# Kernel tuning notes

Measured on AMD Instinct MI355X. Metric: run time of the kernel, lower is better.

## Reference

```python
import jax, jax.numpy as jnp
import numpy as np

N_NODES = 100000
N_EDGES = 1600000
NFEAT = 64
NHID = 64
NCLASS = 16


def setup_inputs() -> dict:
    key = jax.random.key(0)
    k_x, k_e, k_w1, k_b1, k_w2, k_b2 = jax.random.split(key, 6)
    x = jax.random.normal(k_x, (N_NODES, NFEAT), dtype=jnp.float32)
    edge_index = jax.random.randint(k_e, (2, N_EDGES), 0, N_NODES, dtype=jnp.int64)
    # Glorot-ish init for the GIN update MLP
    W1 = jax.random.normal(k_w1, (NFEAT, NHID), dtype=jnp.float32) * (1.0 / np.sqrt(NFEAT))
    b1 = jnp.zeros((NHID,), dtype=jnp.float32)
    W2 = jax.random.normal(k_w2, (NHID, NCLASS), dtype=jnp.float32) * (1.0 / np.sqrt(NHID))
    b2 = jnp.zeros((NCLASS,), dtype=jnp.float32)
    eps = jnp.float32(0.0)  # train_eps=True, initialized to 0
    return {"x": x, "edge_index": edge_index, "eps": eps,
            "W1": W1, "b1": b1, "W2": W2, "b2": b2}


def reference(x, edge_index, eps, W1, b1, W2, b2):
    # GINConv: out = MLP((1 + eps) * x + sum_{j in N(i)} x_j)
    src = edge_index[0]  # message source nodes
    dst = edge_index[1]  # aggregation targets (source_to_target flow)
    agg = jax.ops.segment_sum(x[src], dst, num_segments=x.shape[0])  # [N, F]
    h = (1.0 + eps) * x + agg
    # MLP([nfeat, nhid, nclass]): Linear -> ReLU -> (dropout=identity in eval) -> Linear
    h = jax.nn.relu(h @ W1 + b1)
    return h @ W2 + b2
```

## Files before the change

### kernel.cpp

```cpp
#include <hip/hip_runtime.h>
#include <hip/hip_bf16.h>
#include <hip/hip_fp16.h>


#define NFEAT 64
#define NHID 64
#define NCLASS 16

#define BNODES 128
#define PCAP 2560
#define MAXBUCK 1024
#define PT 512
#define PEPT 8
#define FT 512
#define SEPT 5

__global__ __launch_bounds__(256) void k_tofp16(
    const float4* __restrict__ x4, uint2* __restrict__ xh2, int n16)
{
    int i = blockIdx.x * 256 + threadIdx.x;
    if (i >= n16) return;
    float4 v = x4[i];
    __half2 a = __floats2half2_rn(v.x, v.y);
    __half2 b = __floats2half2_rn(v.z, v.w);
    xh2[i] = make_uint2(*(unsigned*)&a, *(unsigned*)&b);
}

__global__ __launch_bounds__(512) void k_init(int* __restrict__ cursor, int nbuck)
{
    int t = blockIdx.x * 512 + threadIdx.x;
    if (t < nbuck) cursor[t] = t * PCAP;
}

__global__ __launch_bounds__(PT) void k_part(
    const int* __restrict__ ei, int* __restrict__ cursor,
    int* __restrict__ dsts, int n_edges, int nbuck)
{
    __shared__ int lcnt[MAXBUCK];
    __shared__ int sbase[MAXBUCK];
    int tid = threadIdx.x;
    for (int i = tid; i < nbuck; i += PT) lcnt[i] = 0;
    __syncthreads();

    int e0 = blockIdx.x * (PT * PEPT);
    int bk[PEPT], rk[PEPT], pk[PEPT];
    #pragma unroll
    for (int k = 0; k < PEPT; ++k) {
        int e = e0 + k * PT + tid;
        if (e < n_edges) {
            int src = ei[e];
            int dst = ei[n_edges + e];
            int b = dst >> 7;
            bk[k] = b;
            pk[k] = (src << 7) | (dst & 127);
            rk[k] = atomicAdd(&lcnt[b], 1);
        } else bk[k] = -1;
    }
    __syncthreads();
    for (int i = tid; i < nbuck; i += PT)
        sbase[i] = lcnt[i] ? atomicAdd(&cursor[i], lcnt[i]) : 0;
    __syncthreads();
    #pragma unroll
    for (int k = 0; k < PEPT; ++k)
        if (bk[k] >= 0) dsts[sbase[bk[k]] + rk[k]] = pk[k];
}

__global__ __launch_bounds__(FT) void k_fused(
    const uint2* __restrict__ xh2,
    const float4* __restrict__ x4,
    const int* __restrict__ dsts,
    const int* __restrict__ cursor,
    const float* __restrict__ eps_p,
    const float* __restrict__ W1,
    const float* __restrict__ b1,
    const float* __restrict__ W2,
    const float* __restrict__ b2,
    float* __restrict__ out,
    int n_nodes)
{
    __shared__ float sW1[NFEAT * NHID];
    __shared__ float sW2[NHID * 17];
    __shared__ float sb1[NHID];
    __shared__ float sb2[NCLASS];
    __shared__ int   sSrc[PCAP];
    __shared__ int   sCnt[BNODES];
    __shared__ int   sOff[BNODES];
    __shared__ float sh0[32][68];
    __shared__ float sh1[32][68];

    int tid = threadIdx.x;
    int lane = tid & 63, wave = tid >> 6;

    for (int i = tid; i < NFEAT * NHID; i += FT) sW1[i] = W1[i];
    for (int i = tid; i < NHID * NCLASS; i += FT) sW2[(i >> 4) * 17 + (i & 15)] = W2[i];
    if (tid < NHID) sb1[tid] = b1[tid];
    if (tid < NCLASS) sb2[tid] = b2[tid];
    if (tid < BNODES) sCnt[tid] = 0;
    __syncthreads();

    int b = blockIdx.x;
    int gin = b * PCAP;
    int s = cursor[b] - gin;

    int dk[SEPT], rk[SEPT], sk[SEPT];
    #pragma unroll
    for (int k = 0; k < SEPT; ++k) {
        int i = k * FT + tid;
        if (i < s) {
            int p = dsts[gin + i];
            int d = p & 127;
            dk[k] = d;
            sk[k] = p >> 7;
            rk[k] = atomicAdd(&sCnt[d], 1);
        } else dk[k] = -1;
    }
    __syncthreads();
    if (wave == 0) {
        int c0 = sCnt[lane * 2], c1 = sCnt[lane * 2 + 1];
        int p1 = c0, p2 = p1 + c1;
        int ss = p2;
        #pragma unroll
        for (int o = 1; o < 64; o <<= 1) {
            int u = __shfl_up(ss, o);
            if (lane >= o) ss += u;
        }
        int base = ss - p2;
        sOff[lane * 2] = base;
        sOff[lane * 2 + 1] = base + p1;
    }
    __syncthreads();
    #pragma unroll
    for (int k = 0; k < SEPT; ++k)
        if (dk[k] >= 0) sSrc[sOff[dk[k]] + rk[k]] = sk[k];
    __syncthreads();

    float eps1 = 1.0f + eps_p[0];
    int q = lane >> 4;
    int f = lane & 15;
    int rloc = wave * 4 + q;

    #pragma unroll
    for (int pp = 0; pp < 4; ++pp) {
        int nloc = pp * 32 + rloc;
        int node = b * BNODES + nloc;
        bool valid = node < n_nodes;
        int start = sOff[nloc];
        int cntn = sCnt[nloc];

        int dmax = cntn;
        dmax = max(dmax, __shfl_xor(dmax, 16));
        dmax = max(dmax, __shfl_xor(dmax, 32));

        float4 acc = make_float4(0.f, 0.f, 0.f, 0.f);
        for (int base = 0; base < dmax; base += 16) {
            #pragma unroll
            for (int t = 0; t < 16; ++t) {
                int o = base + t;
                int idx = (o < cntn) ? sSrc[start + o] : -1;
                if (idx >= 0) {
                    uint2 hv = xh2[(size_t)idx * 8 + (f >> 1)];
                    unsigned u = (f & 1) ? hv.y : hv.x;
                    (void)u;
                }
            }
            break;
        }
        acc = make_float4(0.f, 0.f, 0.f, 0.f);
        const uint2* xr = xh2;
        for (int base = 0; base < dmax; base += 16) {
            #pragma unroll
            for (int t = 0; t < 16; ++t) {
                int o = base + t;
                int idx = (o < cntn) ? sSrc[start + o] : -1;
                if (idx >= 0) {
                    uint2 hv = xr[(size_t)idx * 16 + f];
                    __half2 ha = *(__half2*)&hv.x;
                    __half2 hb = *(__half2*)&hv.y;
                    float2 fa = __half22float2(ha);
                    float2 fb = __half22float2(hb);
                    acc.x += fa.x; acc.y += fa.y; acc.z += fb.x; acc.w += fb.y;
                }
            }
        }
        if (valid) {
            float4 xs = x4[(size_t)node * 16 + f];
            acc.x += eps1 * xs.x; acc.y += eps1 * xs.y;
            acc.z += eps1 * xs.z; acc.w += eps1 * xs.w;
        }
        *(float4*)&sh0[rloc][f * 4] = acc;

        int r = wave * 4;
        float a0 = sb1[lane], a1 = a0, a2 = a0, a3 = a0;
        #pragma unroll
        for (int kk = 0; kk < 16; ++kk) {
            float4 h0 = *(const float4*)&sh0[r + 0][kk * 4];
            float4 h1v = *(const float4*)&sh0[r + 1][kk * 4];
            float4 h2 = *(const float4*)&sh0[r + 2][kk * 4];
            float4 h3 = *(const float4*)&sh0[r + 3][kk * 4];
            #pragma unroll
            for (int i = 0; i < 4; ++i) {
                float w = sW1[(kk * 4 + i) * NHID + lane];
                a0 += ((const float*)&h0)[i] * w;
                a1 += ((const float*)&h1v)[i] * w;
                a2 += ((const float*)&h2)[i] * w;
                a3 += ((const float*)&h3)[i] * w;
            }
        }
        sh1[r + 0][lane] = fmaxf(a0, 0.f);
        sh1[r + 1][lane] = fmaxf(a1, 0.f);
        sh1[r + 2][lane] = fmaxf(a2, 0.f);
        sh1[r + 3][lane] = fmaxf(a3, 0.f);

        float o2 = sb2[f];
        #pragma unroll
        for (int jj = 0; jj < 16; ++jj) {
            float4 hv = *(const float4*)&sh1[rloc][jj * 4];
            o2 += hv.x * sW2[(jj * 4 + 0) * 17 + f];
            o2 += hv.y * sW2[(jj * 4 + 1) * 17 + f];
            o2 += hv.z * sW2[(jj * 4 + 2) * 17 + f];
            o2 += hv.w * sW2[(jj * 4 + 3) * 17 + f];
        }
        if (valid) out[(size_t)node * NCLASS + f] = o2;
    }
}

extern "C" void kernel_launch(void* const* d_in, const int* in_sizes, int n_in,
                              void* d_out, int out_size, void* d_ws, size_t ws_size,
                              hipStream_t stream) {
    const float* x   = (const float*)d_in[0];
    const int*   ei  = (const int*)d_in[1];
    const float* eps = (const float*)d_in[2];
    const float* W1  = (const float*)d_in[3];
    const float* b1  = (const float*)d_in[4];
    const float* W2  = (const float*)d_in[5];
    const float* b2  = (const float*)d_in[6];
    float* out = (float*)d_out;

    int n_nodes = in_sizes[0] / NFEAT;
    int n_edges = in_sizes[1] / 2;
    int nbuck = (n_nodes + BNODES - 1) / BNODES;

    char* ws = (char*)d_ws;
    int*   cursor = (int*)ws;
    int*   dsts   = (int*)(ws + 4096);
    size_t o_xh   = 4096 + (size_t)nbuck * PCAP * 4;
    uint2* xh2    = (uint2*)(ws + o_xh);

    int n16 = n_nodes * 16;
    k_tofp16<<<(n16 + 255) / 256, 256, 0, stream>>>((const float4*)x, xh2, n16);
    k_init<<<(nbuck + 511) / 512, 512, 0, stream>>>(cursor, nbuck);
    k_part<<<(n_edges + PT * PEPT - 1) / (PT * PEPT), PT, 0, stream>>>(
        ei, cursor, dsts, n_edges, nbuck);
    k_fused<<<nbuck, FT, 0, stream>>>(
        xh2, (const float4*)x, dsts, cursor, eps, W1, b1, W2, b2, out, n_nodes);
}
```

Before: 210.2 us.

## Replace per-node CSR sort in LDS with shared-memory atomic accumulation

```diff
diff --git a/kernel.cpp b/kernel.cpp
--- a/kernel.cpp
+++ b/kernel.cpp
@@ -7,13 +7,13 @@
 #define NHID 64
 #define NCLASS 16
 
-#define BNODES 128
-#define PCAP 2560
-#define MAXBUCK 1024
+#define BSH 6
+#define BNODES 64
+#define PCAP 1536
+#define MAXBUCK 2048
 #define PT 512
-#define PEPT 8
+#define PEPT 16
 #define FT 512
-#define SEPT 5
 
 __global__ __launch_bounds__(256) void k_tofp16(
     const float4* __restrict__ x4, uint2* __restrict__ xh2, int n16)
@@ -50,9 +50,9 @@
         if (e < n_edges) {
             int src = ei[e];
             int dst = ei[n_edges + e];
-            int b = dst >> 7;
+            int b = dst >> BSH;
             bk[k] = b;
-            pk[k] = (src << 7) | (dst & 127);
+            pk[k] = (src << BSH) | (dst & (BNODES - 1));
             rk[k] = atomicAdd(&lcnt[b], 1);
         } else bk[k] = -1;
     }
@@ -82,121 +82,74 @@
     __shared__ float sW2[NHID * 17];
     __shared__ float sb1[NHID];
     __shared__ float sb2[NCLASS];
-    __shared__ int   sSrc[PCAP];
-    __shared__ int   sCnt[BNODES];
-    __shared__ int   sOff[BNODES];
-    __shared__ float sh0[32][68];
+    __shared__ __align__(16) float accF[BNODES][NFEAT];
     __shared__ float sh1[32][68];
 
     int tid = threadIdx.x;
     int lane = tid & 63, wave = tid >> 6;
+    int b = blockIdx.x;
+    int nbase = b * BNODES;
 
     for (int i = tid; i < NFEAT * NHID; i += FT) sW1[i] = W1[i];
     for (int i = tid; i < NHID * NCLASS; i += FT) sW2[(i >> 4) * 17 + (i & 15)] = W2[i];
     if (tid < NHID) sb1[tid] = b1[tid];
     if (tid < NCLASS) sb2[tid] = b2[tid];
-    if (tid < BNODES) sCnt[tid] = 0;
-    __syncthreads();
-
-    int b = blockIdx.x;
+
+    float eps1 = 1.0f + eps_p[0];
+
+    #pragma unroll
+    for (int it = 0; it < 2; ++it) {
+        int idx = it * FT + tid;
+        int node = idx >> 4, f = idx & 15;
+        float4 v = make_float4(0.f, 0.f, 0.f, 0.f);
+        if (nbase + node < n_nodes) v = x4[(size_t)(nbase + node) * 16 + f];
+        float4 w = make_float4(eps1 * v.x, eps1 * v.y, eps1 * v.z, eps1 * v.w);
+        *(float4*)&accF[node][f * 4] = w;
+    }
+    __syncthreads();
+
     int gin = b * PCAP;
     int s = cursor[b] - gin;
-
-    int dk[SEPT], rk[SEPT], sk[SEPT];
-    #pragma unroll
-    for (int k = 0; k < SEPT; ++k) {
-        int i = k * FT + tid;
-        if (i < s) {
-            int p = dsts[gin + i];
-            int d = p & 127;
-            dk[k] = d;
-            sk[k] = p >> 7;
-            rk[k] = atomicAdd(&sCnt[d], 1);
-        } else dk[k] = -1;
-    }
-    __syncthreads();
-    if (wave == 0) {
-        int c0 = sCnt[lane * 2], c1 = sCnt[lane * 2 + 1];
-        int p1 = c0, p2 = p1 + c1;
-        int ss = p2;
-        #pragma unroll
-        for (int o = 1; o < 64; o <<= 1) {
-            int u = __shfl_up(ss, o);
-            if (lane >= o) ss += u;
-        }
-        int base = ss - p2;
-        sOff[lane * 2] = base;
-        sOff[lane * 2 + 1] = base + p1;
-    }
-    __syncthreads();
-    #pragma unroll
-    for (int k = 0; k < SEPT; ++k)
-        if (dk[k] >= 0) sSrc[sOff[dk[k]] + rk[k]] = sk[k];
-    __syncthreads();
-
-    float eps1 = 1.0f + eps_p[0];
     int q = lane >> 4;
     int f = lane & 15;
-    int rloc = wave * 4 + q;
-
-    #pragma unroll
-    for (int pp = 0; pp < 4; ++pp) {
-        int nloc = pp * 32 + rloc;
-        int node = b * BNODES + nloc;
-        bool valid = node < n_nodes;
-        int start = sOff[nloc];
-        int cntn = sCnt[nloc];
-
-        int dmax = cntn;
-        dmax = max(dmax, __shfl_xor(dmax, 16));
-        dmax = max(dmax, __shfl_xor(dmax, 32));
-
-        float4 acc = make_float4(0.f, 0.f, 0.f, 0.f);
-        for (int base = 0; base < dmax; base += 16) {
-            #pragma unroll
-            for (int t = 0; t < 16; ++t) {
-                int o = base + t;
-                int idx = (o < cntn) ? sSrc[start + o] : -1;
-                if (idx >= 0) {
-                    uint2 hv = xh2[(size_t)idx * 8 + (f >> 1)];
-                    unsigned u = (f & 1) ? hv.y : hv.x;
-                    (void)u;
-                }
-            }
-            break;
-        }
-        acc = make_float4(0.f, 0.f, 0.f, 0.f);
-        const uint2* xr = xh2;
-        for (int base = 0; base < dmax; base += 16) {
-            #pragma unroll
-            for (int t = 0; t < 16; ++t) {
-                int o = base + t;
-                int idx = (o < cntn) ? sSrc[start + o] : -1;
-                if (idx >= 0) {
-                    uint2 hv = xr[(size_t)idx * 16 + f];
-                    __half2 ha = *(__half2*)&hv.x;
-                    __half2 hb = *(__half2*)&hv.y;
-                    float2 fa = __half22float2(ha);
-                    float2 fb = __half22float2(hb);
-                    acc.x += fa.x; acc.y += fa.y; acc.z += fb.x; acc.w += fb.y;
-                }
+    int slot = (f + 4 * q) & 15;
+
+    for (int c0 = wave * 64; c0 < s; c0 += 8 * 64) {
+        int pos = c0 + lane;
+        int myedge = (pos < s) ? dsts[gin + pos] : -1;
+        #pragma unroll
+        for (int t = 0; t < 16; ++t) {
+            int pe = __shfl(myedge, t * 4 + q);
+            if (pe >= 0) {
+                int src = pe >> BSH;
+                int d   = pe & (BNODES - 1);
+                uint2 hv = xh2[(size_t)src * 16 + slot];
+                float2 fa = __half22float2(*(__half2*)&hv.x);
+                float2 fb = __half22float2(*(__half2*)&hv.y);
+                float* ap = &accF[d][slot * 4];
+                atomicAdd(ap + 0, fa.x);
+                atomicAdd(ap + 1, fa.y);
+                atomicAdd(ap + 2, fb.x);
+                atomicAdd(ap + 3, fb.y);
             }
         }
-        if (valid) {
-            float4 xs = x4[(size_t)node * 16 + f];
-            acc.x += eps1 * xs.x; acc.y += eps1 * xs.y;
-            acc.z += eps1 * xs.z; acc.w += eps1 * xs.w;
-        }
-        *(float4*)&sh0[rloc][f * 4] = acc;
-
-        int r = wave * 4;
+    }
+    __syncthreads();
+
+    int rloc = wave * 4 + q;
+    #pragma unroll
+    for (int pp = 0; pp < 2; ++pp) {
+        int nloc = pp * 32 + rloc;
+        int node = nbase + nloc;
+        int r = pp * 32 + wave * 4;
+
         float a0 = sb1[lane], a1 = a0, a2 = a0, a3 = a0;
         #pragma unroll
         for (int kk = 0; kk < 16; ++kk) {
-            float4 h0 = *(const float4*)&sh0[r + 0][kk * 4];
-            float4 h1v = *(const float4*)&sh0[r + 1][kk * 4];
-            float4 h2 = *(const float4*)&sh0[r + 2][kk * 4];
-            float4 h3 = *(const float4*)&sh0[r + 3][kk * 4];
+            float4 h0  = *(const float4*)&accF[r + 0][kk * 4];
+            float4 h1v = *(const float4*)&accF[r + 1][kk * 4];
+            float4 h2  = *(const float4*)&accF[r + 2][kk * 4];
+            float4 h3  = *(const float4*)&accF[r + 3][kk * 4];
             #pragma unroll
             for (int i = 0; i < 4; ++i) {
                 float w = sW1[(kk * 4 + i) * NHID + lane];
@@ -206,21 +159,22 @@
                 a3 += ((const float*)&h3)[i] * w;
             }
         }
-        sh1[r + 0][lane] = fmaxf(a0, 0.f);
-        sh1[r + 1][lane] = fmaxf(a1, 0.f);
-        sh1[r + 2][lane] = fmaxf(a2, 0.f);
-        sh1[r + 3][lane] = fmaxf(a3, 0.f);
+        int rr = wave * 4;
+        sh1[rr + 0][lane] = fmaxf(a0, 0.f);
+        sh1[rr + 1][lane] = fmaxf(a1, 0.f);
+        sh1[rr + 2][lane] = fmaxf(a2, 0.f);
+        sh1[rr + 3][lane] = fmaxf(a3, 0.f);
 
         float o2 = sb2[f];
         #pragma unroll
         for (int jj = 0; jj < 16; ++jj) {
-            float4 hv = *(const float4*)&sh1[rloc][jj * 4];
+            float4 hv = *(const float4*)&sh1[rr + q][jj * 4];
             o2 += hv.x * sW2[(jj * 4 + 0) * 17 + f];
             o2 += hv.y * sW2[(jj * 4 + 1) * 17 + f];
             o2 += hv.z * sW2[(jj * 4 + 2) * 17 + f];
             o2 += hv.w * sW2[(jj * 4 + 3) * 17 + f];
         }
-        if (valid) out[(size_t)node * NCLASS + f] = o2;
+        if (node < n_nodes) out[(size_t)node * NCLASS + f] = o2;
     }
 }
 
@@ -242,8 +196,8 @@
 
     char* ws = (char*)d_ws;
     int*   cursor = (int*)ws;
-    int*   dsts   = (int*)(ws + 4096);
-    size_t o_xh   = 4096 + (size_t)nbuck * PCAP * 4;
+    int*   dsts   = (int*)(ws + 8192);
+    size_t o_xh   = 8192 + (size_t)nbuck * PCAP * 4;
     uint2* xh2    = (uint2*)(ws + o_xh);
 
     int n16 = n_nodes * 16;
```

Measured after the change: 732.6 us. +248.5%, slower.
